# Kernel optimization log

Hardware: AMD Instinct MI355X
Metric: run time of the kernel (lower is better)

The kernel has to match this reference:

```python
import jax, jax.numpy as jnp
import numpy as np

L, H, D, HD, DFF, V, S, B = 12, 12, 768, 64, 3072, 50257, 512, 4
NEG = -1e10  # mask value used by the torch module (applied incl. diagonal, pre-scale)


def layer_norm(x, g, b, eps=1e-5):
    u = jnp.mean(x, axis=-1, keepdims=True)
    v = jnp.mean((x - u) ** 2, axis=-1, keepdims=True)  # biased variance
    return g * (x - u) / jnp.sqrt(v + eps) + b


def setup_inputs() -> dict:
    key = jax.random.key(0)
    ks = jax.random.split(key, 10)
    f = lambda k, s: 0.02 * jax.random.normal(k, s, dtype=jnp.float32)
    return {
        "tokens": jax.random.randint(ks[0], (B, S), 0, V),
        "E": f(ks[1], (V, D)),
        "P": f(ks[2], (S, D)),
        "Wq": f(ks[3], (L, H, HD, D)),
        "Wk": f(ks[4], (L, H, HD, D)),
        "Wv": f(ks[5], (L, H, HD, D)),
        "Wo": f(ks[6], (L, D, D)),
        "bo": jnp.zeros((L, D), jnp.float32),
        "g1": jnp.ones((L, D), jnp.float32),
        "b1": jnp.zeros((L, D), jnp.float32),
        "g2": jnp.ones((L, D), jnp.float32),
        "b2": jnp.zeros((L, D), jnp.float32),
        "W1": f(ks[7], (L, DFF, D)),
        "bff1": jnp.zeros((L, DFF), jnp.float32),
        "W2": f(ks[8], (L, D, DFF)),
        "bff2": jnp.zeros((L, D), jnp.float32),
        "gf": jnp.ones((D,), jnp.float32),
        "bf": jnp.zeros((D,), jnp.float32),
    }


def reference(tokens, E, P, Wq, Wk, Wv, Wo, bo, g1, b1, g2, b2, W1, bff1, W2, bff2, gf, bf):
    x = E[tokens] + P[None, :, :]  # [B,S,D]; embed_dropout is identity at eval
    # Faithful mask: triu with diagonal=0 (masks the diagonal too), added BEFORE 1/sqrt(dk)
    mask = jnp.triu(jnp.ones((S, S), jnp.float32), k=0) * NEG
    scale = 1.0 / jnp.sqrt(jnp.float32(HD))
    for l in range(L):
        h = layer_norm(x, g1[l], b1[l])
        Q = jnp.einsum('bsd,hkd->bhsk', h, Wq[l])
        K = jnp.einsum('bsd,hkd->bhsk', h, Wk[l])
        Vh = jnp.einsum('bsd,hkd->bhsk', h, Wv[l])
        sc = (jnp.einsum('bhqk,bhmk->bhqm', Q, K) + mask) * scale  # [B,H,S,S]
        A = jax.nn.softmax(sc, axis=-1)
        o = jnp.einsum('bhqm,bhmk->bhqk', A, Vh)  # [B,H,S,HD]
        o = o.transpose(0, 2, 1, 3).reshape(B, S, D)  # concat heads
        x = x + jnp.einsum('bsd,ed->bse', o, Wo[l]) + bo[l]
        h2 = layer_norm(x, g2[l], b2[l])
        ff = jax.nn.gelu(jnp.einsum('bsd,fd->bsf', h2, W1[l]) + bff1[l], approximate=False)
        x = x + jnp.einsum('bsf,df->bsd', ff, W2[l]) + bff2[l]
    x = layer_norm(x, gf, bf)
    return jnp.einsum('bsd,vd->bsv', x, E)  # weight-tied LM head
```

## Files before the change

### kernel.cpp

```cpp
#include <hip/hip_runtime.h>
#include <hip/hip_bf16.h>
#include <math.h>
#include <stdint.h>

#define L      12
#define H      12
#define DMODEL 768
#define HDIM   64
#define DFF    3072
#define VOCAB  50257
#define VPAD   50304
#define SEQ    512
#define BATCH  4
#define MTOK   2048

typedef __hip_bfloat16 bf16;
typedef __bf16 bf16x8 __attribute__((ext_vector_type(8)));
typedef float  f32x4  __attribute__((ext_vector_type(4)));

__device__ inline float bfbits2f(unsigned int u) {
    return __builtin_bit_cast(float, u << 16);
}
__device__ inline unsigned int f2bf_bits(float f) {
    __hip_bfloat16 h = __float2bfloat16(f);
    return (unsigned int)__builtin_bit_cast(unsigned short, h);
}

typedef __attribute__((address_space(1))) unsigned int as1_uint;
typedef __attribute__((address_space(3))) unsigned int as3_uint;

__device__ inline void load_lds_16B(const void* g, void* l) {
    __builtin_amdgcn_global_load_lds((as1_uint*)(uintptr_t)g,
                                     (as3_uint*)(uintptr_t)l, 16, 0, 0);
}

__device__ inline int xcd_swz(int raw, int nwg) {
    return (raw & 7) * (nwg >> 3) + (raw >> 3);
}

__global__ void cvt_pad_kernel(bf16* __restrict__ dst, const float* __restrict__ src,
                               long ns, long nt) {
    long i8 = ((long)blockIdx.x * blockDim.x + threadIdx.x) * 8;
    long stride = (long)gridDim.x * blockDim.x * 8;
    for (; i8 < nt; i8 += stride) {
        uint4 out;
        if (i8 < ns) {
            float4 a = *reinterpret_cast<const float4*>(src + i8);
            float4 b = *reinterpret_cast<const float4*>(src + i8 + 4);
            out.x = f2bf_bits(a.x) | (f2bf_bits(a.y) << 16);
            out.y = f2bf_bits(a.z) | (f2bf_bits(a.w) << 16);
            out.z = f2bf_bits(b.x) | (f2bf_bits(b.y) << 16);
            out.w = f2bf_bits(b.z) | (f2bf_bits(b.w) << 16);
        } else {
            out = (uint4){0u, 0u, 0u, 0u};
        }
        *reinterpret_cast<uint4*>(dst + i8) = out;
    }
}

__global__ __launch_bounds__(256) void embed_ln_kernel(
        float* __restrict__ x, bf16* __restrict__ hout,
        const int* __restrict__ tok, const float* __restrict__ E,
        const float* __restrict__ P, const float* __restrict__ g,
        const float* __restrict__ b) {
    int row = blockIdx.x, tid = threadIdx.x;
    int s = row % SEQ;
    size_t ebase = (size_t)tok[row] * DMODEL;
    float v[3];
    #pragma unroll
    for (int e = 0; e < 3; e++) {
        int c = tid + e * 256;
        v[e] = E[ebase + c] + P[s * DMODEL + c];
        x[(size_t)row * DMODEL + c] = v[e];
    }
    float s1 = v[0] + v[1] + v[2];
    float s2 = v[0] * v[0] + v[1] * v[1] + v[2] * v[2];
    #pragma unroll
    for (int o = 32; o > 0; o >>= 1) {
        s1 += __shfl_down(s1, o);
        s2 += __shfl_down(s2, o);
    }
    __shared__ float w1[4], w2[4];
    int wv = tid >> 6;
    if ((tid & 63) == 0) { w1[wv] = s1; w2[wv] = s2; }
    __syncthreads();
    s1 = w1[0] + w1[1] + w1[2] + w1[3];
    s2 = w2[0] + w2[1] + w2[2] + w2[3];
    float u    = s1 * (1.f / DMODEL);
    float var  = s2 * (1.f / DMODEL) - u * u;
    float rstd = rsqrtf(var + 1e-5f);
    size_t base = (size_t)row * DMODEL;
    #pragma unroll
    for (int e = 0; e < 3; e++) {
        int c = tid + e * 256;
        hout[base + c] = __float2bfloat16(g[c] * (v[e] - u) * rstd + b[c]);
    }
}

__global__ __launch_bounds__(256) void reduce_ln_kernel(
        float* __restrict__ x, const float* __restrict__ part, int S,
        const float* __restrict__ bias, const float* __restrict__ g,
        const float* __restrict__ b, bf16* __restrict__ hout) {
    int row = blockIdx.x, tid = threadIdx.x;
    float v[3];
    #pragma unroll
    for (int e = 0; e < 3; e++) {
        int c = tid + e * 256;
        size_t idx = (size_t)row * DMODEL + c;
        float acc = x[idx] + bias[c];
        for (int s = 0; s < S; s++)
            acc += part[((size_t)s * MTOK + row) * DMODEL + c];
        v[e] = acc;
        x[idx] = acc;
    }
    float s1 = v[0] + v[1] + v[2];
    float s2 = v[0] * v[0] + v[1] * v[1] + v[2] * v[2];
    #pragma unroll
    for (int o = 32; o > 0; o >>= 1) {
        s1 += __shfl_down(s1, o);
        s2 += __shfl_down(s2, o);
    }
    __shared__ float w1[4], w2[4];
    int wv = tid >> 6;
    if ((tid & 63) == 0) { w1[wv] = s1; w2[wv] = s2; }
    __syncthreads();
    s1 = w1[0] + w1[1] + w1[2] + w1[3];
    s2 = w2[0] + w2[1] + w2[2] + w2[3];
    float u    = s1 * (1.f / DMODEL);
    float var  = s2 * (1.f / DMODEL) - u * u;
    float rstd = rsqrtf(var + 1e-5f);
    size_t base = (size_t)row * DMODEL;
    #pragma unroll
    for (int e = 0; e < 3; e++) {
        int c = tid + e * 256;
        hout[base + c] = __float2bfloat16(g[c] * (v[e] - u) * rstd + b[c]);
    }
}

#define BM 128
#define BKK 64

template<int BN_, int EPI>
__global__ __launch_bounds__(256) void gemm_bt(
    const bf16* __restrict__ A, const bf16* __restrict__ Bmat, long strideBz,
    void* __restrict__ Cout, long strideCz,
    const float* __restrict__ bias,
    int Mm, int Nn, int Kk, int Nstore, int kslice)
{
    constexpr int NF = BN_ / 32;
    __shared__ __align__(16) bf16 As[2][BM * BKK];
    __shared__ __align__(16) bf16 Bs[2][BN_ * BKK];
    int tid = threadIdx.x;
    int lane = tid & 63, wave = tid >> 6;

    int Mtiles = Mm / BM;
    int id = xcd_swz(blockIdx.x, gridDim.x);
    int bm = (id % Mtiles) * BM;
    int bn = (id / Mtiles) * BN_;
    int z = blockIdx.z;
    const bf16* Bz = Bmat + (size_t)z * strideBz;
    int wr = (wave >> 1) * 64, wc = (wave & 1) * (BN_ / 2);

    int k0 = (EPI == 4) ? z * kslice : 0;
    int nt = ((EPI == 4) ? kslice : Kk) / BKK;

    f32x4 acc[4][NF];
    #pragma unroll
    for (int i = 0; i < 4; i++)
        #pragma unroll
        for (int j = 0; j < NF; j++) acc[i][j] = (f32x4){0.f, 0.f, 0.f, 0.f};

    auto stage = [&](int buf, int kt) {
        #pragma unroll
        for (int i = 0; i < 4; i++) {
            int byte = i * 4096 + tid * 16;
            int r = byte >> 7;
            int scb = (byte & 127) ^ ((r & 7) << 4);
            load_lds_16B(A + (size_t)(bm + r) * Kk + kt + (scb >> 1),
                         (char*)As[buf] + byte);
        }
        #pragma unroll
        for (int i = 0; i < BN_ / 32; i++) {
            int byte = i * 4096 + tid * 16;
            int r = byte >> 7;
            int scb = (byte & 127) ^ ((r & 7) << 4);
            load_lds_16B(Bz + (size_t)(bn + r) * Kk + kt + (scb >> 1),
                         (char*)Bs[buf] + byte);
        }
    };

    stage(0, k0);
    __syncthreads();

    const int swz_rd = (lane & 7) << 4;
    int cur = 0;
    for (int t = 0; t < nt; ++t) {
        if (t + 1 < nt) stage(cur ^ 1, k0 + (t + 1) * BKK);
        #pragma unroll
        for (int kk = 0; kk < 2; ++kk) {
            bf16x8 af[4], bfr[NF];
            int ro = lane & 15;
            int cob = kk * 64 + (lane >> 4) * 16;
            #pragma unroll
            for (int mi = 0; mi < 4; mi++) {
                int row = wr + mi * 16 + ro;
                af[mi] = *reinterpret_cast<const bf16x8*>(
                    (const char*)As[cur] + row * 128 + (cob ^ swz_rd));
            }
            #pragma unroll
            for (int ni = 0; ni < NF; ni++) {
                int row = wc + ni * 16 + ro;
                bfr[ni] = *reinterpret_cast<const bf16x8*>(
                    (const char*)Bs[cur] + row * 128 + (cob ^ swz_rd));
            }
            #pragma unroll
            for (int mi = 0; mi < 4; mi++)
                #pragma unroll
                for (int ni = 0; ni < NF; ni++)
                    acc[mi][ni] = __builtin_amdgcn_mfma_f32_16x16x32_bf16(
                        af[mi], bfr[ni], acc[mi][ni], 0, 0, 0);
        }
        __syncthreads();
        cur ^= 1;
    }

    int rbase = bm + wr + ((lane >> 4) << 2);
    int cbase = bn + wc + (lane & 15);
    #pragma unroll
    for (int mi = 0; mi < 4; mi++) {
        #pragma unroll
        for (int ni = 0; ni < NF; ni++) {
            int col = cbase + ni * 16;
            #pragma unroll
            for (int r = 0; r < 4; r++) {
                int row = rbase + mi * 16 + r;
                float v = acc[mi][ni][r];
                if constexpr (EPI == 0) {
                    ((bf16*)Cout)[(size_t)z * strideCz + (size_t)row * Nn + col] =
                        __float2bfloat16(v);
                } else if constexpr (EPI == 2) {
                    float t = v + bias[col];
                    float gel = 0.5f * t * (1.f + erff(t * 0.70710678118654752f));
                    ((bf16*)Cout)[(size_t)row * Nn + col] = __float2bfloat16(gel);
                } else if constexpr (EPI == 3) {
                    if (col < Nstore)
                        ((float*)Cout)[(size_t)row * Nstore + col] = v;
                } else {
                    ((float*)Cout)[(size_t)z * strideCz + (size_t)row * Nn + col] = v;
                }
            }
        }
    }
}

#define NEGMASK -1e10f
#define SM_SCALE 0.125f

__global__ __launch_bounds__(256) void attn_kernel(
    bf16* __restrict__ o, const bf16* __restrict__ qb,
    const bf16* __restrict__ kb, const bf16* __restrict__ vb)
{
    __shared__ __align__(16) bf16 K_lds[64 * 64];
    __shared__ __align__(16) bf16 VT_lds[64 * 64];
    __shared__ __align__(16) bf16 P_lds[4][16 * 64];

    int tid = threadIdx.x;
    int wave = tid >> 6, lane = tid & 63;
    int g = lane >> 4;
    int cq = lane & 15;
    int idx = xcd_swz(blockIdx.x, gridDim.x);
    int qt = idx & 7;
    int bh = idx >> 3;
    int h = bh % H, b = bh / H;
    int q0 = qt * 64;
    const size_t base = ((size_t)b * SEQ) * DMODEL + h * HDIM;

    bf16x8 qa[2];
    #pragma unroll
    for (int kk = 0; kk < 2; kk++)
        qa[kk] = *reinterpret_cast<const bf16x8*>(
            qb + base + (size_t)(q0 + wave * 16 + cq) * DMODEL + kk * 32 + g * 8);

    f32x4 acc_o[4];
    #pragma unroll
    for (int df = 0; df < 4; df++) acc_o[df] = (f32x4){0.f, 0.f, 0.f, 0.f};
    float m_run[4] = {-INFINITY, -INFINITY, -INFINITY, -INFINITY};
    float l_run[4] = {0.f, 0.f, 0.f, 0.f};

    int ntiles = (qt == 0) ? (SEQ / 64) : (qt + 1);
    for (int t = 0; t < ntiles; ++t) {
        int mt = t * 64;
        __syncthreads();
        #pragma unroll
        for (int i = 0; i < 2; i++) {
            int byte = i * 4096 + tid * 16;
            int r = byte >> 7;
            int scb = (byte & 127) ^ ((r & 7) << 4);
            load_lds_16B(kb + base + (size_t)(mt + r) * DMODEL + (scb >> 1),
                         (char*)K_lds + byte);
        }
        {
            int rp = tid & 31;
            int c0 = (tid >> 5) * 8;
            const bf16* v0p = vb + base + (size_t)(mt + 2 * rp) * DMODEL + c0;
            uint4 a = *reinterpret_cast<const uint4*>(v0p);
            uint4 bb = *reinterpret_cast<const uint4*>(v0p + DMODEL);
            unsigned int au[4] = {a.x, a.y, a.z, a.w};
            unsigned int bu[4] = {bb.x, bb.y, bb.z, bb.w};
            #pragma unroll
            for (int j = 0; j < 8; j++) {
                unsigned int lo = (j & 1) ? (au[j >> 1] >> 16) : (au[j >> 1] & 0xffffu);
                unsigned int hi = (j & 1) ? (bu[j >> 1] >> 16) : (bu[j >> 1] & 0xffffu);
                int d = c0 + j;
                int byte = d * 128 + ((rp * 4) ^ ((d & 7) << 4));
                *reinterpret_cast<unsigned int*>((char*)VT_lds + byte) = lo | (hi << 16);
            }
        }
        __syncthreads();

        f32x4 s[4];
        #pragma unroll
        for (int nf = 0; nf < 4; nf++) s[nf] = (f32x4){0.f, 0.f, 0.f, 0.f};
        #pragma unroll
        for (int kk = 0; kk < 2; kk++) {
            #pragma unroll
            for (int nf = 0; nf < 4; nf++) {
                int row = nf * 16 + cq;
                bf16x8 kf = *reinterpret_cast<const bf16x8*>(
                    (const char*)K_lds + row * 128 +
                    ((kk * 64 + g * 16) ^ ((row & 7) << 4)));
                s[nf] = __builtin_amdgcn_mfma_f32_16x16x32_bf16(qa[kk], kf, s[nf], 0, 0, 0);
            }
        }

        float p[4][4];
        #pragma unroll
        for (int r = 0; r < 4; r++) {
            int qg = q0 + wave * 16 + (g << 2) + r;
            float sv[4];
            float vmax = -INFINITY;
            #pragma unroll
            for (int nf = 0; nf < 4; nf++) {
                int kv = mt + nf * 16 + cq;
                float d = s[nf][r];
                sv[nf] = (kv >= qg) ? (d + NEGMASK) * SM_SCALE : d * SM_SCALE;
                vmax = fmaxf(vmax, sv[nf]);
            }
            vmax = fmaxf(vmax, __shfl_xor(vmax, 1));
            vmax = fmaxf(vmax, __shfl_xor(vmax, 2));
            vmax = fmaxf(vmax, __shfl_xor(vmax, 4));
            vmax = fmaxf(vmax, __shfl_xor(vmax, 8));
            float nm = fmaxf(m_run[r], vmax);
            float f = __expf(m_run[r] - nm);
            m_run[r] = nm;
            float ps = 0.f;
            #pragma unroll
            for (int nf = 0; nf < 4; nf++) {
                float pv = __expf(sv[nf] - nm);
                p[nf][r] = pv;
                ps += pv;
            }
            ps += __shfl_xor(ps, 1);
            ps += __shfl_xor(ps, 2);
            ps += __shfl_xor(ps, 4);
            ps += __shfl_xor(ps, 8);
            l_run[r] = l_run[r] * f + ps;
            #pragma unroll
            for (int df = 0; df < 4; df++) acc_o[df][r] *= f;
        }

        #pragma unroll
        for (int nf = 0; nf < 4; nf++)
            #pragma unroll
            for (int r = 0; r < 4; r++) {
                int q = (g << 2) + r;
                int blog = nf * 32 + cq * 2;
                int byte = wave * 2048 + q * 128 + (blog ^ ((q & 7) << 4));
                *reinterpret_cast<unsigned short*>((char*)P_lds + byte) =
                    (unsigned short)f2bf_bits(p[nf][r]);
            }
        __syncthreads();

        #pragma unroll
        for (int kk = 0; kk < 2; kk++) {
            bf16x8 pa = *reinterpret_cast<const bf16x8*>(
                (const char*)P_lds + wave * 2048 + cq * 128 +
                ((kk * 64 + g * 16) ^ ((cq & 7) << 4)));
            #pragma unroll
            for (int df = 0; df < 4; df++) {
                int row = df * 16 + cq;
                bf16x8 vf = *reinterpret_cast<const bf16x8*>(
                    (const char*)VT_lds + row * 128 +
                    ((kk * 64 + g * 16) ^ ((row & 7) << 4)));
                acc_o[df] = __builtin_amdgcn_mfma_f32_16x16x32_bf16(pa, vf, acc_o[df], 0, 0, 0);
            }
        }
    }

    #pragma unroll
    for (int r = 0; r < 4; r++) {
        float inv = 1.f / l_run[r];
        int qg = q0 + wave * 16 + (g << 2) + r;
        #pragma unroll
        for (int df = 0; df < 4; df++) {
            o[base + (size_t)qg * DMODEL + df * 16 + cq] =
                __float2bfloat16(acc_o[df][r] * inv);
        }
    }
}

extern "C" void kernel_launch(void* const* d_in, const int* in_sizes, int n_in,
                              void* d_out, int out_size, void* d_ws, size_t ws_size,
                              hipStream_t stream)
{
    (void)in_sizes; (void)n_in; (void)out_size; (void)ws_size;
    const int*   tokens = (const int*)d_in[0];
    const float* E    = (const float*)d_in[1];
    const float* P    = (const float*)d_in[2];
    const float* Wq   = (const float*)d_in[3];
    const float* Wk   = (const float*)d_in[4];
    const float* Wv   = (const float*)d_in[5];
    const float* Wo   = (const float*)d_in[6];
    const float* bo   = (const float*)d_in[7];
    const float* g1   = (const float*)d_in[8];
    const float* b1   = (const float*)d_in[9];
    const float* g2   = (const float*)d_in[10];
    const float* b2   = (const float*)d_in[11];
    const float* W1   = (const float*)d_in[12];
    const float* bff1 = (const float*)d_in[13];
    const float* W2   = (const float*)d_in[14];
    const float* bff2 = (const float*)d_in[15];
    const float* gf   = (const float*)d_in[16];
    const float* bfin = (const float*)d_in[17];

    char* ws = (char*)d_ws;
    size_t off = 0;
    auto alloc = [&](size_t bytes) -> void* {
        void* p = ws + off;
        off += (bytes + 255) & ~(size_t)255;
        return p;
    };
    float* x     = (float*)alloc((size_t)MTOK * DMODEL * 4);
    bf16* hbuf   = (bf16*)alloc((size_t)MTOK * DMODEL * 2);
    bf16* qkv    = (bf16*)alloc((size_t)3 * MTOK * DMODEL * 2);
    bf16* obuf   = (bf16*)alloc((size_t)MTOK * DMODEL * 2);
    bf16* ffb    = (bf16*)alloc((size_t)MTOK * DFF * 2);
    float* part  = (float*)alloc((size_t)3 * MTOK * DMODEL * 4);
    bf16* Eb     = (bf16*)alloc((size_t)VPAD * DMODEL * 2);
    bf16* Wqkv_b = (bf16*)alloc((size_t)3 * L * DMODEL * DMODEL * 2);
    bf16* Wo_b   = (bf16*)alloc((size_t)L * DMODEL * DMODEL * 2);
    bf16* W1_b   = (bf16*)alloc((size_t)L * DFF * DMODEL * 2);
    bf16* W2_b   = (bf16*)alloc((size_t)L * DMODEL * DFF * 2);

    long nE  = (long)VOCAB * DMODEL;
    long nEp = (long)VPAD * DMODEL;
    cvt_pad_kernel<<<2048, 256, 0, stream>>>(Eb, E, nE, nEp);
    long nW = (long)L * DMODEL * DMODEL;
    cvt_pad_kernel<<<2048, 256, 0, stream>>>(Wqkv_b,          Wq, nW, nW);
    cvt_pad_kernel<<<2048, 256, 0, stream>>>(Wqkv_b + nW,     Wk, nW, nW);
    cvt_pad_kernel<<<2048, 256, 0, stream>>>(Wqkv_b + 2 * nW, Wv, nW, nW);
    cvt_pad_kernel<<<2048, 256, 0, stream>>>(Wo_b,            Wo, nW, nW);
    long nF = (long)L * DFF * DMODEL;
    cvt_pad_kernel<<<2048, 256, 0, stream>>>(W1_b, W1, nF, nF);
    cvt_pad_kernel<<<2048, 256, 0, stream>>>(W2_b, W2, nF, nF);

    embed_ln_kernel<<<MTOK, 256, 0, stream>>>(x, hbuf, tokens, E, P, g1, b1);

    const long pstride = (long)MTOK * DMODEL;
    for (int l = 0; l < L; ++l) {
        gemm_bt<64, 0><<<dim3(16 * 12, 1, 3), 256, 0, stream>>>(
            hbuf, Wqkv_b + (size_t)l * DMODEL * DMODEL, (long)L * DMODEL * DMODEL,
            qkv, pstride, nullptr, MTOK, DMODEL, DMODEL, 0, 0);
        attn_kernel<<<BATCH * H * (SEQ / 64), 256, 0, stream>>>(
            obuf, qkv, qkv + pstride, qkv + 2 * pstride);
        gemm_bt<64, 4><<<dim3(16 * 12, 1, 3), 256, 0, stream>>>(
            obuf, Wo_b + (size_t)l * DMODEL * DMODEL, 0,
            part, pstride, nullptr, MTOK, DMODEL, DMODEL, 0, DMODEL / 3);
        reduce_ln_kernel<<<MTOK, 256, 0, stream>>>(
            x, part, 3, bo + l * DMODEL, g2 + l * DMODEL, b2 + l * DMODEL, hbuf);
        gemm_bt<64, 2><<<dim3(16 * 48, 1, 1), 256, 0, stream>>>(
            hbuf, W1_b + (size_t)l * DFF * DMODEL, 0,
            ffb, 0, bff1 + l * DFF, MTOK, DFF, DMODEL, 0, 0);
        gemm_bt<64, 4><<<dim3(16 * 12, 1, 3), 256, 0, stream>>>(
            ffb, W2_b + (size_t)l * DMODEL * DFF, 0,
            part, pstride, nullptr, MTOK, DMODEL, DFF, 0, DFF / 3);
        const float* ng = (l < L - 1) ? (g1 + (l + 1) * DMODEL) : gf;
        const float* nb = (l < L - 1) ? (b1 + (l + 1) * DMODEL) : bfin;
        reduce_ln_kernel<<<MTOK, 256, 0, stream>>>(
            x, part, 3, bff2 + l * DMODEL, ng, nb, hbuf);
    }
    gemm_bt<128, 3><<<dim3(16 * 393, 1, 1), 256, 0, stream>>>(
        hbuf, Eb, 0, d_out, 0, nullptr, MTOK, VPAD, DMODEL, VOCAB, 0);
}
```

Before: 1.736 ms.

## Triple-buffer GEMM LDS pipeline with vmcnt waits, nontemporal stores, BN=64 LM head

Replaces the double-buffered GEMM mainloop with a three-slot ring. Two tiles are prefetched ahead, and each iteration waits with an explicit s_waitcnt vmcnt plus a single barrier instead of two __syncthreads. This should hide global-to-LDS latency better. It also fixes BN at 64, so the LM-head GEMM now runs with twice as many blocks and narrower tiles. Fp32 partial and logit outputs use nontemporal stores and the reduce kernel uses nontemporal loads to reduce cache pollution. Risks are the extra LDS per block, which lowers occupancy, and a correctness risk if nt is 1, since the kernel always stages two tiles.

```diff
diff --git a/kernel.cpp b/kernel.cpp
--- a/kernel.cpp
+++ b/kernel.cpp
@@ -109,7 +109,8 @@
         size_t idx = (size_t)row * DMODEL + c;
         float acc = x[idx] + bias[c];
         for (int s = 0; s < S; s++)
-            acc += part[((size_t)s * MTOK + row) * DMODEL + c];
+            acc += __builtin_nontemporal_load(
+                &part[((size_t)s * MTOK + row) * DMODEL + c]);
         v[e] = acc;
         x[idx] = acc;
     }
@@ -138,28 +139,29 @@
 }
 
 #define BM 128
+#define BN 64
 #define BKK 64
 
-template<int BN_, int EPI>
+template<int EPI>
 __global__ __launch_bounds__(256) void gemm_bt(
     const bf16* __restrict__ A, const bf16* __restrict__ Bmat, long strideBz,
     void* __restrict__ Cout, long strideCz,
     const float* __restrict__ bias,
     int Mm, int Nn, int Kk, int Nstore, int kslice)
 {
-    constexpr int NF = BN_ / 32;
-    __shared__ __align__(16) bf16 As[2][BM * BKK];
-    __shared__ __align__(16) bf16 Bs[2][BN_ * BKK];
+    constexpr int NF = BN / 32;
+    __shared__ __align__(16) bf16 As[3][BM * BKK];
+    __shared__ __align__(16) bf16 Bs[3][BN * BKK];
     int tid = threadIdx.x;
     int lane = tid & 63, wave = tid >> 6;
 
     int Mtiles = Mm / BM;
     int id = xcd_swz(blockIdx.x, gridDim.x);
     int bm = (id % Mtiles) * BM;
-    int bn = (id / Mtiles) * BN_;
+    int bn = (id / Mtiles) * BN;
     int z = blockIdx.z;
     const bf16* Bz = Bmat + (size_t)z * strideBz;
-    int wr = (wave >> 1) * 64, wc = (wave & 1) * (BN_ / 2);
+    int wr = (wave >> 1) * 64, wc = (wave & 1) * (BN / 2);
 
     int k0 = (EPI == 4) ? z * kslice : 0;
     int nt = ((EPI == 4) ? kslice : Kk) / BKK;
@@ -170,32 +172,39 @@
         #pragma unroll
         for (int j = 0; j < NF; j++) acc[i][j] = (f32x4){0.f, 0.f, 0.f, 0.f};
 
-    auto stage = [&](int buf, int kt) {
+    auto stage = [&](int slot, int kt) {
         #pragma unroll
         for (int i = 0; i < 4; i++) {
             int byte = i * 4096 + tid * 16;
             int r = byte >> 7;
             int scb = (byte & 127) ^ ((r & 7) << 4);
             load_lds_16B(A + (size_t)(bm + r) * Kk + kt + (scb >> 1),
-                         (char*)As[buf] + byte);
-        }
-        #pragma unroll
-        for (int i = 0; i < BN_ / 32; i++) {
+                         (char*)As[slot] + byte);
+        }
+        #pragma unroll
+        for (int i = 0; i < 2; i++) {
             int byte = i * 4096 + tid * 16;
             int r = byte >> 7;
             int scb = (byte & 127) ^ ((r & 7) << 4);
             load_lds_16B(Bz + (size_t)(bn + r) * Kk + kt + (scb >> 1),
-                         (char*)Bs[buf] + byte);
+                         (char*)Bs[slot] + byte);
         }
     };
 
     stage(0, k0);
-    __syncthreads();
+    stage(1, k0 + BKK);
 
     const int swz_rd = (lane & 7) << 4;
-    int cur = 0;
     for (int t = 0; t < nt; ++t) {
-        if (t + 1 < nt) stage(cur ^ 1, k0 + (t + 1) * BKK);
+        if (t < nt - 1) {
+            asm volatile("s_waitcnt vmcnt(6)" ::: "memory");
+        } else {
+            asm volatile("s_waitcnt vmcnt(0)" ::: "memory");
+        }
+        __builtin_amdgcn_s_barrier();
+        __builtin_amdgcn_sched_barrier(0);
+        if (t + 2 < nt) stage((t + 2) % 3, k0 + (t + 2) * BKK);
+        int cur = t % 3;
         #pragma unroll
         for (int kk = 0; kk < 2; ++kk) {
             bf16x8 af[4], bfr[NF];
@@ -220,8 +229,6 @@
                     acc[mi][ni] = __builtin_amdgcn_mfma_f32_16x16x32_bf16(
                         af[mi], bfr[ni], acc[mi][ni], 0, 0, 0);
         }
-        __syncthreads();
-        cur ^= 1;
     }
 
     int rbase = bm + wr + ((lane >> 4) << 2);
@@ -244,9 +251,11 @@
                     ((bf16*)Cout)[(size_t)row * Nn + col] = __float2bfloat16(gel);
                 } else if constexpr (EPI == 3) {
                     if (col < Nstore)
-                        ((float*)Cout)[(size_t)row * Nstore + col] = v;
+                        __builtin_nontemporal_store(v,
+                            &((float*)Cout)[(size_t)row * Nstore + col]);
                 } else {
-                    ((float*)Cout)[(size_t)z * strideCz + (size_t)row * Nn + col] = v;
+                    __builtin_nontemporal_store(v,
+                        &((float*)Cout)[(size_t)z * strideCz + (size_t)row * Nn + col]);
                 }
             }
         }
@@ -468,20 +477,20 @@
 
     const long pstride = (long)MTOK * DMODEL;
     for (int l = 0; l < L; ++l) {
-        gemm_bt<64, 0><<<dim3(16 * 12, 1, 3), 256, 0, stream>>>(
+        gemm_bt<0><<<dim3(16 * 12, 1, 3), 256, 0, stream>>>(
             hbuf, Wqkv_b + (size_t)l * DMODEL * DMODEL, (long)L * DMODEL * DMODEL,
             qkv, pstride, nullptr, MTOK, DMODEL, DMODEL, 0, 0);
         attn_kernel<<<BATCH * H * (SEQ / 64), 256, 0, stream>>>(
             obuf, qkv, qkv + pstride, qkv + 2 * pstride);
-        gemm_bt<64, 4><<<dim3(16 * 12, 1, 3), 256, 0, stream>>>(
+        gemm_bt<4><<<dim3(16 * 12, 1, 3), 256, 0, stream>>>(
             obuf, Wo_b + (size_t)l * DMODEL * DMODEL, 0,
             part, pstride, nullptr, MTOK, DMODEL, DMODEL, 0, DMODEL / 3);
         reduce_ln_kernel<<<MTOK, 256, 0, stream>>>(
             x, part, 3, bo + l * DMODEL, g2 + l * DMODEL, b2 + l * DMODEL, hbuf);
-        gemm_bt<64, 2><<<dim3(16 * 48, 1, 1), 256, 0, stream>>>(
+        gemm_bt<2><<<dim3(16 * 48, 1, 1), 256, 0, stream>>>(
             hbuf, W1_b + (size_t)l * DFF * DMODEL, 0,
             ffb, 0, bff1 + l * DFF, MTOK, DFF, DMODEL, 0, 0);
-        gemm_bt<64, 4><<<dim3(16 * 12, 1, 3), 256, 0, stream>>>(
+        gemm_bt<4><<<dim3(16 * 12, 1, 3), 256, 0, stream>>>(
             ffb, W2_b + (size_t)l * DMODEL * DFF, 0,
             part, pstride, nullptr, MTOK, DMODEL, DFF, 0, DFF / 3);
         const float* ng = (l < L - 1) ? (g1 + (l + 1) * DMODEL) : gf;
@@ -489,6 +498,6 @@
         reduce_ln_kernel<<<MTOK, 256, 0, stream>>>(
             x, part, 3, bff2 + l * DMODEL, ng, nb, hbuf);
     }
-    gemm_bt<128, 3><<<dim3(16 * 393, 1, 1), 256, 0, stream>>>(
+    gemm_bt<3><<<dim3(16 * 786, 1, 1), 256, 0, stream>>>(
         hbuf, Eb, 0, d_out, 0, nullptr, MTOK, VPAD, DMODEL, VOCAB, 0);
 }
```

Result: slower. 2.039 ms (+17.5%).

## Add triple-buffered LDS ring with explicit vmcnt waits to GEMM; retile FF1 and LM head

Applied to the files above, without the earlier changes.

Restructures the GEMM main loop. BN=64 kernels now use a three-slot LDS ring that prefetches two tiles ahead, synchronised with explicit s_waitcnt vmcnt and raw s_barrier instead of __syncthreads. BN=128 kernels keep double buffering but also use explicit vmcnt waits. The FF1 GEMM switches to BN=128 tiles, and the vocab padding grows to a multiple of 128 columns so the LM-head grid covers it (394 column tiles). The risks are higher LDS use per block, which can lower occupancy, and hand-counted vmcnt values that must match the number of issued loads exactly.

```diff
diff --git a/kernel.cpp b/kernel.cpp
--- a/kernel.cpp
+++ b/kernel.cpp
@@ -9,7 +9,7 @@
 #define HDIM   64
 #define DFF    3072
 #define VOCAB  50257
-#define VPAD   50304
+#define VPAD2  50432
 #define SEQ    512
 #define BATCH  4
 #define MTOK   2048
@@ -147,9 +147,11 @@
     const float* __restrict__ bias,
     int Mm, int Nn, int Kk, int Nstore, int kslice)
 {
+    constexpr int RING = (BN_ == 128) ? 2 : 3;
     constexpr int NF = BN_ / 32;
-    __shared__ __align__(16) bf16 As[2][BM * BKK];
-    __shared__ __align__(16) bf16 Bs[2][BN_ * BKK];
+    constexpr int LOADS = 4 + BN_ / 32;
+    __shared__ __align__(16) bf16 As[RING][BM * BKK];
+    __shared__ __align__(16) bf16 Bs[RING][BN_ * BKK];
     int tid = threadIdx.x;
     int lane = tid & 63, wave = tid >> 6;
 
@@ -170,14 +172,14 @@
         #pragma unroll
         for (int j = 0; j < NF; j++) acc[i][j] = (f32x4){0.f, 0.f, 0.f, 0.f};
 
-    auto stage = [&](int buf, int kt) {
+    auto stage = [&](int slot, int kt) {
         #pragma unroll
         for (int i = 0; i < 4; i++) {
             int byte = i * 4096 + tid * 16;
             int r = byte >> 7;
             int scb = (byte & 127) ^ ((r & 7) << 4);
             load_lds_16B(A + (size_t)(bm + r) * Kk + kt + (scb >> 1),
-                         (char*)As[buf] + byte);
+                         (char*)As[slot] + byte);
         }
         #pragma unroll
         for (int i = 0; i < BN_ / 32; i++) {
@@ -185,17 +187,12 @@
             int r = byte >> 7;
             int scb = (byte & 127) ^ ((r & 7) << 4);
             load_lds_16B(Bz + (size_t)(bn + r) * Kk + kt + (scb >> 1),
-                         (char*)Bs[buf] + byte);
+                         (char*)Bs[slot] + byte);
         }
     };
 
-    stage(0, k0);
-    __syncthreads();
-
     const int swz_rd = (lane & 7) << 4;
-    int cur = 0;
-    for (int t = 0; t < nt; ++t) {
-        if (t + 1 < nt) stage(cur ^ 1, k0 + (t + 1) * BKK);
+    auto compute = [&](int cur) {
         #pragma unroll
         for (int kk = 0; kk < 2; ++kk) {
             bf16x8 af[4], bfr[NF];
@@ -220,8 +217,36 @@
                     acc[mi][ni] = __builtin_amdgcn_mfma_f32_16x16x32_bf16(
                         af[mi], bfr[ni], acc[mi][ni], 0, 0, 0);
         }
-        __syncthreads();
-        cur ^= 1;
+    };
+
+    if constexpr (RING == 3) {
+        stage(0, k0);
+        stage(1, k0 + BKK);
+        for (int t = 0; t < nt; ++t) {
+            if (t < nt - 1) {
+                asm volatile("s_waitcnt vmcnt(6)" ::: "memory");
+            } else {
+                asm volatile("s_waitcnt vmcnt(0)" ::: "memory");
+            }
+            __builtin_amdgcn_s_barrier();
+            __builtin_amdgcn_sched_barrier(0);
+            if (t + 2 < nt) stage((t + 2) % 3, k0 + (t + 2) * BKK);
+            compute(t % 3);
+        }
+    } else {
+        stage(0, k0);
+        for (int t = 0; t < nt; ++t) {
+            if (t + 1 < nt) {
+                stage((t + 1) & 1, k0 + (t + 1) * BKK);
+                asm volatile("s_waitcnt vmcnt(8)" ::: "memory");
+            } else {
+                asm volatile("s_waitcnt vmcnt(0)" ::: "memory");
+            }
+            __builtin_amdgcn_s_barrier();
+            __builtin_amdgcn_sched_barrier(0);
+            compute(t & 1);
+            __builtin_amdgcn_s_barrier();
+        }
     }
 
     int rbase = bm + wr + ((lane >> 4) << 2);
@@ -446,14 +471,14 @@
     bf16* obuf   = (bf16*)alloc((size_t)MTOK * DMODEL * 2);
     bf16* ffb    = (bf16*)alloc((size_t)MTOK * DFF * 2);
     float* part  = (float*)alloc((size_t)3 * MTOK * DMODEL * 4);
-    bf16* Eb     = (bf16*)alloc((size_t)VPAD * DMODEL * 2);
+    bf16* Eb     = (bf16*)alloc((size_t)VPAD2 * DMODEL * 2);
     bf16* Wqkv_b = (bf16*)alloc((size_t)3 * L * DMODEL * DMODEL * 2);
     bf16* Wo_b   = (bf16*)alloc((size_t)L * DMODEL * DMODEL * 2);
     bf16* W1_b   = (bf16*)alloc((size_t)L * DFF * DMODEL * 2);
     bf16* W2_b   = (bf16*)alloc((size_t)L * DMODEL * DFF * 2);
 
     long nE  = (long)VOCAB * DMODEL;
-    long nEp = (long)VPAD * DMODEL;
+    long nEp = (long)VPAD2 * DMODEL;
     cvt_pad_kernel<<<2048, 256, 0, stream>>>(Eb, E, nE, nEp);
     long nW = (long)L * DMODEL * DMODEL;
     cvt_pad_kernel<<<2048, 256, 0, stream>>>(Wqkv_b,          Wq, nW, nW);
@@ -478,7 +503,7 @@
             part, pstride, nullptr, MTOK, DMODEL, DMODEL, 0, DMODEL / 3);
         reduce_ln_kernel<<<MTOK, 256, 0, stream>>>(
             x, part, 3, bo + l * DMODEL, g2 + l * DMODEL, b2 + l * DMODEL, hbuf);
-        gemm_bt<64, 2><<<dim3(16 * 48, 1, 1), 256, 0, stream>>>(
+        gemm_bt<128, 2><<<dim3(16 * 24, 1, 1), 256, 0, stream>>>(
             hbuf, W1_b + (size_t)l * DFF * DMODEL, 0,
             ffb, 0, bff1 + l * DFF, MTOK, DFF, DMODEL, 0, 0);
         gemm_bt<64, 4><<<dim3(16 * 12, 1, 3), 256, 0, stream>>>(
@@ -489,6 +514,6 @@
         reduce_ln_kernel<<<MTOK, 256, 0, stream>>>(
             x, part, 3, bff2 + l * DMODEL, ng, nb, hbuf);
     }
-    gemm_bt<128, 3><<<dim3(16 * 393, 1, 1), 256, 0, stream>>>(
-        hbuf, Eb, 0, d_out, 0, nullptr, MTOK, VPAD, DMODEL, VOCAB, 0);
-}
+    gemm_bt<128, 3><<<dim3(16 * 394, 1, 1), 256, 0, stream>>>(
+        hbuf, Eb, 0, d_out, 0, nullptr, MTOK, VPAD2, DMODEL, VOCAB, 0);
+}
```

New measurement: 1.810 ms. 4.2% more time.
